# Optimization experiments

Hardware: AMD Instinct MI355X
Metric: run time of the kernel (lower is better)

The kernel has to match this reference:

```python
import jax, jax.numpy as jnp
import numpy as np

B, C_IN, C_OUT, H, K = 64, 64, 128, 1855, 6


def setup_inputs() -> dict:
    key = jax.random.key(0)
    k1, k2, k3, k4 = jax.random.split(key, 4)
    x = jax.random.normal(k1, (B, C_IN, H), dtype=jnp.float32)
    # neighbor table [H, K]; valid indices first, -1 padding at the end
    neighbors = jax.random.randint(k2, (H, K), 0, H)
    n_boundary = H // 10
    neighbors = neighbors.at[:n_boundary, K - 2:].set(-1)
    weight_center = jax.random.normal(k3, (C_OUT, C_IN), dtype=jnp.float32) / np.sqrt(C_IN).astype(np.float32)
    weight_neighbors = jax.random.normal(k4, (C_OUT, C_IN, K), dtype=jnp.float32) / np.sqrt(C_IN * K).astype(np.float32)
    bias = jnp.zeros((C_OUT,), dtype=jnp.float32)
    return {
        "x": x,
        "neighbors": neighbors,
        "weight_center": weight_center,
        "weight_neighbors": weight_neighbors,
        "bias": bias,
    }


def reference(x, neighbors, weight_center, weight_neighbors, bias):
    # x: [B, C_in, H]; neighbors: [H, K] with -1 = invalid (valid-first ordering)
    mask = neighbors >= 0                               # [H, K]
    idx = jnp.where(mask, neighbors, 0)                 # safe gather indices
    gathered = x[:, :, idx] * mask.astype(x.dtype)[None, None, :, :]  # [B, C_in, H, K]
    center = jnp.einsum('bch,oc->boh', x, weight_center)              # [B, C_out, H]
    neigh = jnp.einsum('bchk,ock->boh', gathered, weight_neighbors)   # [B, C_out, H]
    counts = (1 + mask.sum(axis=-1)).astype(x.dtype)                  # [H]
    return (center + neigh) / counts[None, None, :] + bias[None, :, None]
```

## Files before the change

kernel.cpp:

```cpp
#include <hip/hip_runtime.h>
#include <stdint.h>

typedef __bf16 bf16x8 __attribute__((ext_vector_type(8)));
typedef float floatx4 __attribute__((ext_vector_type(4)));
typedef unsigned int u32x4 __attribute__((ext_vector_type(4)));
typedef unsigned short u16;
typedef unsigned int u32;

#define CIN   64
#define COUT  128
#define H_    1855
#define KNB   6
#define KTOT  448
#define NSTEPS 14

#define HLROW 2064
#define BUFSZ 33024
#define STCP  36

#define WP_OFF   ((size_t)H_ * 4096 * 2)
#define CINV_OFF (WP_OFF + (size_t)COUT * KTOT * 2)
#define ZERO_OFF (CINV_OFF + 7424)

#define PIN4(v) asm volatile("" : "+v"(v))

typedef __attribute__((address_space(1))) unsigned int as1_u32;
typedef __attribute__((address_space(3))) unsigned int as3_u32;
static __device__ __forceinline__ void ld16_to_lds(const void* g, void* l) {
    __builtin_amdgcn_global_load_lds((const as1_u32*)g, (as3_u32*)l, 16, 0, 0);
}

static __device__ inline u16 f32_to_bf16(float f) {
    u32 u = __float_as_uint(f);
    u32 r = (u + 0x7FFFu + ((u >> 16) & 1u)) >> 16;
    return (u16)r;
}

__global__ __launch_bounds__(256) void k_transpose(const float* __restrict__ x,
                                                   u16* __restrict__ xt3) {
    __shared__ u16 tile[64][65];
    int h0  = blockIdx.x * 64;
    int bc0 = blockIdx.y * 64;
    int lane = threadIdx.x & 63;
    int rowq = threadIdx.x >> 6;
    int h = h0 + lane;
    bool hv = h < H_;
#pragma unroll
    for (int i = 0; i < 16; ++i) {
        int row = i * 4 + rowq;
        u16 v = 0;
        if (hv) v = f32_to_bf16(x[(size_t)(bc0 + row) * H_ + h]);
        tile[row][lane] = v;
    }
    __syncthreads();
#pragma unroll
    for (int i = 0; i < 16; ++i) {
        int hr = i * 4 + rowq;
        int hh = h0 + hr;
        if (hh < H_) xt3[(size_t)hh * 4096 + bc0 + lane] = tile[lane][hr];
    }
}

__global__ __launch_bounds__(256) void k_pack(const float* __restrict__ wc,
                                              const float* __restrict__ wn,
                                              const int* __restrict__ nbr,
                                              u16* __restrict__ wp,
                                              float* __restrict__ cInvG,
                                              u32* __restrict__ zeroPg) {
    int tg = blockIdx.x * 256 + threadIdx.x;
    if (tg < 64) zeroPg[tg] = 0u;
    if (tg < H_) {
        int cnt = 1;
#pragma unroll
        for (int j = 0; j < KNB; ++j) cnt += (nbr[tg * KNB + j] >= 0) ? 1 : 0;
        cInvG[tg] = 1.0f / (float)cnt;
    }
    if (tg >= COUT * KTOT) return;
    int o = tg / KTOT;
    int rem = tg - o * KTOT;
    int s = rem >> 6, c = rem & 63;
    float v = (s == 0) ? wc[o * CIN + c]
                       : wn[(o * CIN + c) * KNB + (s - 1)];
    wp[tg] = f32_to_bf16(v);
}

static __device__ __forceinline__ void stage_tile(
    const u16* __restrict__ xt3, const int* __restrict__ nbr,
    const char* __restrict__ zeroPg, char* bufB,
    int h0t, int b0, int wave, int lane) {
    int lane16 = lane & 15;
    int ssub   = lane >> 4;
    int bl     = lane16 >> 3;
    int chunk  = lane16 & 7;
#pragma unroll
    for (int i = 0; i < 8; ++i) {
        int hlL = i & 3;
        int sg  = i >> 2;
        int hl  = wave * 4 + hlL;
        int s   = sg * 4 + ssub;
        int hh  = h0t + hl;
        int hcl = hh < H_ ? hh : 0;
        int sidx = (s >= 1 && s <= 6) ? (s - 1) : 0;
        int nv  = nbr[hcl * KNB + sidx];
        int src = (s == 0) ? hcl : nv;
        bool valid = (hh < H_) && (s <= 6) && (src >= 0);
        const char* gp = valid
            ? (const char*)(xt3 + (size_t)src * 4096 + (b0 + bl) * 64 + chunk * 8)
            : (zeroPg + lane16 * 16);
        ld16_to_lds(gp, bufB + hl * HLROW + sg * 1024);
    }
}

__global__ __launch_bounds__(256, 2) void k_main(const u16* __restrict__ xt3,
                                                 const u16* __restrict__ wp,
                                                 const int* __restrict__ nbr,
                                                 const float* __restrict__ bias,
                                                 const float* __restrict__ cInvG,
                                                 const char* __restrict__ zeroPg,
                                                 float* __restrict__ out) {
    __shared__ __align__(16) char LDS[2 * BUFSZ];

    int tid  = threadIdx.x;
    int g    = blockIdx.x;
    int bp   = g & 31;
    int hs   = g >> 5;
    int b0   = bp * 2;
    int h0   = hs * 64;

    int lane = tid & 63;
    int wave = tid >> 6;
    int col  = lane & 15;
    int quad = lane >> 4;
    int m0w  = wave * 32;

    u32x4 afrag[2][NSTEPS];
#pragma unroll
    for (int mt = 0; mt < 2; ++mt) {
        int o = m0w + mt * 16 + col;
#pragma unroll
        for (int kk = 0; kk < NSTEPS; ++kk)
            afrag[mt][kk] = *(const u32x4*)(wp + o * KTOT + kk * 32 + quad * 8);
    }
#pragma unroll
    for (int mt = 0; mt < 2; ++mt)
#pragma unroll
        for (int kk = 0; kk < NSTEPS; ++kk)
            PIN4(afrag[mt][kk]);

    float biasv[2][4];
#pragma unroll
    for (int mt = 0; mt < 2; ++mt)
#pragma unroll
        for (int r = 0; r < 4; ++r)
            biasv[mt][r] = bias[m0w + mt * 16 + quad * 4 + r];

    int rb0 = col * HLROW + quad * 16;
    int rb1 = rb0 + 128;

    stage_tile(xt3, nbr, zeroPg, LDS, h0, b0, wave, lane);

#pragma unroll
    for (int tt = 0; tt < 4; ++tt) {
        int h0t = h0 + tt * 16;
        char* cur = LDS + (tt & 1) * BUFSZ;

        __syncthreads();

        if (tt < 3)
            stage_tile(xt3, nbr, zeroPg, LDS + ((tt + 1) & 1) * BUFSZ,
                       h0t + 16, b0, wave, lane);

        floatx4 acc[2][2];
#pragma unroll
        for (int mt = 0; mt < 2; ++mt)
#pragma unroll
            for (int nt = 0; nt < 2; ++nt)
                acc[mt][nt] = (floatx4){0.0f, 0.0f, 0.0f, 0.0f};

#pragma unroll
        for (int kk = 0; kk < NSTEPS; ++kk) {
            int koff = (kk >> 1) * 256 + (kk & 1) * 64;
            bf16x8 bf0 = *(const bf16x8*)(cur + rb0 + koff);
            bf16x8 bf1 = *(const bf16x8*)(cur + rb1 + koff);
            bf16x8 a0 = __builtin_bit_cast(bf16x8, afrag[0][kk]);
            bf16x8 a1 = __builtin_bit_cast(bf16x8, afrag[1][kk]);
            acc[0][0] = __builtin_amdgcn_mfma_f32_16x16x32_bf16(a0, bf0, acc[0][0], 0, 0, 0);
            acc[1][0] = __builtin_amdgcn_mfma_f32_16x16x32_bf16(a1, bf0, acc[1][0], 0, 0, 0);
            acc[0][1] = __builtin_amdgcn_mfma_f32_16x16x32_bf16(a0, bf1, acc[0][1], 0, 0, 0);
            acc[1][1] = __builtin_amdgcn_mfma_f32_16x16x32_bf16(a1, bf1, acc[1][1], 0, 0, 0);
        }

        __syncthreads();

        float* stC = (float*)cur;
        int hEp = h0t + col;
        float ic = cInvG[hEp < H_ ? hEp : 0];
#pragma unroll
        for (int mt = 0; mt < 2; ++mt)
#pragma unroll
            for (int nt = 0; nt < 2; ++nt)
#pragma unroll
                for (int r = 0; r < 4; ++r) {
                    int o = m0w + mt * 16 + quad * 4 + r;
                    stC[o * STCP + nt * 16 + col] = acc[mt][nt][r] * ic + biasv[mt][r];
                }
        int n5 = lane & 31, q2 = lane >> 5;
        int colS = n5 & 15, ntS = n5 >> 4;
        int hS = h0t + colS;
        bool hv = hS < H_;
        size_t obase = ((size_t)(b0 + ntS) * COUT) * H_ + hS;
#pragma unroll
        for (int rr = 0; rr < 16; ++rr) {
            int o = m0w + rr * 2 + q2;
            if (hv) out[obase + (size_t)o * H_] = stC[o * STCP + n5];
        }
    }
}

extern "C" void kernel_launch(void* const* d_in, const int* in_sizes, int n_in,
                              void* d_out, int out_size, void* d_ws, size_t ws_size,
                              hipStream_t stream) {
    const float* x    = (const float*)d_in[0];
    const int*   nbr  = (const int*)d_in[1];
    const float* wc   = (const float*)d_in[2];
    const float* wn   = (const float*)d_in[3];
    const float* bias = (const float*)d_in[4];

    u16*   xt3    = (u16*)d_ws;
    u16*   wp     = (u16*)((char*)d_ws + WP_OFF);
    float* cInvG  = (float*)((char*)d_ws + CINV_OFF);
    u32*   zeroPg = (u32*)((char*)d_ws + ZERO_OFF);

    k_pack<<<dim3((COUT * KTOT + 255) / 256), dim3(256), 0, stream>>>(
        wc, wn, nbr, wp, cInvG, zeroPg);
    k_transpose<<<dim3(29, 64), dim3(256), 0, stream>>>(x, xt3);
    k_main<<<dim3(928), dim3(256), 0, stream>>>(
        xt3, wp, nbr, bias, cInvG, (const char*)zeroPg, (float*)d_out);
}
```

Baseline: 140.3 us.

## Precompute gather offsets, hand-schedule staging with partial waits, vectorize transpose stores

k_pack now builds a per-hexagon table of byte offsets for the center and neighbor rows, with a sentinel for invalid entries, so k_main no longer computes gather addresses from the neighbor table inside its loop. k_main preloads all offsets and inverse counts into registers. It runs an explicit software pipeline with manual waitcnt barriers, including a partial vmcnt wait that keeps the next stage's loads in flight, raises wave priority around the MFMA loop, and batches the epilogue over two tiles through a swizzled LDS staging area for wider coalesced output stores. The transpose kernel now writes 16-byte vectors instead of 2-byte stores. The cost is higher register pressure and fragile hand-written waitcnt counts.

```diff
diff --git a/kernel.cpp b/kernel.cpp
--- a/kernel.cpp
+++ b/kernel.cpp
@@ -5,6 +5,7 @@
 typedef float floatx4 __attribute__((ext_vector_type(4)));
 typedef unsigned int u32x4 __attribute__((ext_vector_type(4)));
 typedef unsigned short u16;
+typedef unsigned short u16x8 __attribute__((ext_vector_type(8)));
 typedef unsigned int u32;
 
 #define CIN   64
@@ -16,11 +17,12 @@
 
 #define HLROW 2064
 #define BUFSZ 33024
-#define STCP  36
-
-#define WP_OFF   ((size_t)H_ * 4096 * 2)
-#define CINV_OFF (WP_OFF + (size_t)COUT * KTOT * 2)
-#define ZERO_OFF (CINV_OFF + 7424)
+
+#define WP_OFF     ((size_t)H_ * 4096 * 2)
+#define CINV_OFF   (WP_OFF + (size_t)COUT * KTOT * 2)
+#define ZERO_OFF   (CINV_OFF + 7424)
+#define SRCOFF_OFF (ZERO_OFF + 1024)
+#define INVOFF 0xFFFFFFFFu
 
 #define PIN4(v) asm volatile("" : "+v"(v))
 
@@ -41,8 +43,9 @@
     __shared__ u16 tile[64][65];
     int h0  = blockIdx.x * 64;
     int bc0 = blockIdx.y * 64;
-    int lane = threadIdx.x & 63;
-    int rowq = threadIdx.x >> 6;
+    int tid  = threadIdx.x;
+    int lane = tid & 63;
+    int rowq = tid >> 6;
     int h = h0 + lane;
     bool hv = h < H_;
 #pragma unroll
@@ -53,11 +56,17 @@
         tile[row][lane] = v;
     }
     __syncthreads();
-#pragma unroll
-    for (int i = 0; i < 16; ++i) {
-        int hr = i * 4 + rowq;
-        int hh = h0 + hr;
-        if (hh < H_) xt3[(size_t)hh * 4096 + bc0 + lane] = tile[lane][hr];
+    int bg = tid & 7;
+    int hb = tid >> 3;
+#pragma unroll
+    for (int ii = 0; ii < 2; ++ii) {
+        int hl = ii * 32 + hb;
+        int hh = h0 + hl;
+        u16x8 v;
+#pragma unroll
+        for (int j = 0; j < 8; ++j) v[j] = tile[bg * 8 + j][hl];
+        if (hh < H_)
+            *(u16x8*)(xt3 + (size_t)hh * 4096 + bc0 + bg * 8) = v;
     }
 }
 
@@ -66,7 +75,8 @@
                                               const int* __restrict__ nbr,
                                               u16* __restrict__ wp,
                                               float* __restrict__ cInvG,
-                                              u32* __restrict__ zeroPg) {
+                                              u32* __restrict__ zeroPg,
+                                              u32* __restrict__ srcOff) {
     int tg = blockIdx.x * 256 + threadIdx.x;
     if (tg < 64) zeroPg[tg] = 0u;
     if (tg < H_) {
@@ -74,6 +84,16 @@
 #pragma unroll
         for (int j = 0; j < KNB; ++j) cnt += (nbr[tg * KNB + j] >= 0) ? 1 : 0;
         cInvG[tg] = 1.0f / (float)cnt;
+    }
+    if (tg < H_ * 8) {
+        int h = tg >> 3, s = tg & 7;
+        u32 e;
+        if (s == 0) e = (u32)h * 8192u;
+        else if (s <= 6) {
+            int n = nbr[h * KNB + (s - 1)];
+            e = (n >= 0) ? (u32)n * 8192u : INVOFF;
+        } else e = INVOFF;
+        srcOff[tg] = e;
     }
     if (tg >= COUT * KTOT) return;
     int o = tg / KTOT;
@@ -84,46 +104,18 @@
     wp[tg] = f32_to_bf16(v);
 }
 
-static __device__ __forceinline__ void stage_tile(
-    const u16* __restrict__ xt3, const int* __restrict__ nbr,
-    const char* __restrict__ zeroPg, char* bufB,
-    int h0t, int b0, int wave, int lane) {
-    int lane16 = lane & 15;
-    int ssub   = lane >> 4;
-    int bl     = lane16 >> 3;
-    int chunk  = lane16 & 7;
-#pragma unroll
-    for (int i = 0; i < 8; ++i) {
-        int hlL = i & 3;
-        int sg  = i >> 2;
-        int hl  = wave * 4 + hlL;
-        int s   = sg * 4 + ssub;
-        int hh  = h0t + hl;
-        int hcl = hh < H_ ? hh : 0;
-        int sidx = (s >= 1 && s <= 6) ? (s - 1) : 0;
-        int nv  = nbr[hcl * KNB + sidx];
-        int src = (s == 0) ? hcl : nv;
-        bool valid = (hh < H_) && (s <= 6) && (src >= 0);
-        const char* gp = valid
-            ? (const char*)(xt3 + (size_t)src * 4096 + (b0 + bl) * 64 + chunk * 8)
-            : (zeroPg + lane16 * 16);
-        ld16_to_lds(gp, bufB + hl * HLROW + sg * 1024);
-    }
-}
-
 __global__ __launch_bounds__(256, 2) void k_main(const u16* __restrict__ xt3,
                                                  const u16* __restrict__ wp,
-                                                 const int* __restrict__ nbr,
                                                  const float* __restrict__ bias,
                                                  const float* __restrict__ cInvG,
-                                                 const char* __restrict__ zeroPg,
+                                                 const u32* __restrict__ srcOff,
                                                  float* __restrict__ out) {
     __shared__ __align__(16) char LDS[2 * BUFSZ];
 
     int tid  = threadIdx.x;
-    int g    = blockIdx.x;
-    int bp   = g & 31;
-    int hs   = g >> 5;
+    int gbl  = blockIdx.x;
+    int bp   = gbl & 31;
+    int hs   = gbl >> 5;
     int b0   = bp * 2;
     int h0   = hs * 64;
 
@@ -132,6 +124,12 @@
     int col  = lane & 15;
     int quad = lane >> 4;
     int m0w  = wave * 32;
+    int lane16 = lane & 15;
+    int ssub = lane >> 4;
+    int bl   = lane16 >> 3;
+    int chunk = lane16 & 7;
+
+    const char* xb = (const char*)xt3;
 
     u32x4 afrag[2][NSTEPS];
 #pragma unroll
@@ -154,67 +152,117 @@
         for (int r = 0; r < 4; ++r)
             biasv[mt][r] = bias[m0w + mt * 16 + quad * 4 + r];
 
+    float icv[4];
+#pragma unroll
+    for (int t = 0; t < 4; ++t) {
+        int hic = h0 + t * 16 + col;
+        icv[t] = cInvG[hic < H_ ? hic : 0];
+    }
+
+    u32 colOff = (u32)((b0 + bl) * 128 + chunk * 16);
+    u32 zOff   = (u32)ZERO_OFF + (u32)(lane16 * 16);
+    u32 offs[4][8];
+#pragma unroll
+    for (int t = 0; t < 4; ++t)
+#pragma unroll
+        for (int i = 0; i < 8; ++i) {
+            int hh = h0 + t * 16 + wave * 4 + (i & 3);
+            int s  = (i >> 2) * 4 + ssub;
+            u32 e = (hh < H_) ? srcOff[hh * 8 + s] : INVOFF;
+            offs[t][i] = (e == INVOFF) ? zOff : (e + colOff);
+        }
+
     int rb0 = col * HLROW + quad * 16;
     int rb1 = rb0 + 128;
-
-    stage_tile(xt3, nbr, zeroPg, LDS, h0, b0, wave, lane);
-
-#pragma unroll
-    for (int tt = 0; tt < 4; ++tt) {
-        int h0t = h0 + tt * 16;
-        char* cur = LDS + (tt & 1) * BUFSZ;
-
-        __syncthreads();
-
-        if (tt < 3)
-            stage_tile(xt3, nbr, zeroPg, LDS + ((tt + 1) & 1) * BUFSZ,
-                       h0t + 16, b0, wave, lane);
-
-        floatx4 acc[2][2];
-#pragma unroll
-        for (int mt = 0; mt < 2; ++mt)
-#pragma unroll
-            for (int nt = 0; nt < 2; ++nt)
-                acc[mt][nt] = (floatx4){0.0f, 0.0f, 0.0f, 0.0f};
-
-#pragma unroll
-        for (int kk = 0; kk < NSTEPS; ++kk) {
-            int koff = (kk >> 1) * 256 + (kk & 1) * 64;
-            bf16x8 bf0 = *(const bf16x8*)(cur + rb0 + koff);
-            bf16x8 bf1 = *(const bf16x8*)(cur + rb1 + koff);
-            bf16x8 a0 = __builtin_bit_cast(bf16x8, afrag[0][kk]);
-            bf16x8 a1 = __builtin_bit_cast(bf16x8, afrag[1][kk]);
-            acc[0][0] = __builtin_amdgcn_mfma_f32_16x16x32_bf16(a0, bf0, acc[0][0], 0, 0, 0);
-            acc[1][0] = __builtin_amdgcn_mfma_f32_16x16x32_bf16(a1, bf0, acc[1][0], 0, 0, 0);
-            acc[0][1] = __builtin_amdgcn_mfma_f32_16x16x32_bf16(a0, bf1, acc[0][1], 0, 0, 0);
-            acc[1][1] = __builtin_amdgcn_mfma_f32_16x16x32_bf16(a1, bf1, acc[1][1], 0, 0, 0);
-        }
-
-        __syncthreads();
-
-        float* stC = (float*)cur;
-        int hEp = h0t + col;
-        float ic = cInvG[hEp < H_ ? hEp : 0];
-#pragma unroll
-        for (int mt = 0; mt < 2; ++mt)
-#pragma unroll
-            for (int nt = 0; nt < 2; ++nt)
-#pragma unroll
-                for (int r = 0; r < 4; ++r) {
-                    int o = m0w + mt * 16 + quad * 4 + r;
-                    stC[o * STCP + nt * 16 + col] = acc[mt][nt][r] * ic + biasv[mt][r];
-                }
-        int n5 = lane & 31, q2 = lane >> 5;
-        int colS = n5 & 15, ntS = n5 >> 4;
-        int hS = h0t + colS;
-        bool hv = hS < H_;
-        size_t obase = ((size_t)(b0 + ntS) * COUT) * H_ + hS;
-#pragma unroll
-        for (int rr = 0; rr < 16; ++rr) {
-            int o = m0w + rr * 2 + q2;
-            if (hv) out[obase + (size_t)o * H_] = stC[o * STCP + n5];
-        }
-    }
+    char* buf0 = LDS;
+    char* buf1 = LDS + BUFSZ;
+    float* E = (float*)(LDS + BUFSZ);
+
+#define STAGE(t, bufp) do {                                                   \
+    char* _d = (bufp) + (wave * 4) * HLROW;                                   \
+    _Pragma("unroll")                                                         \
+    for (int _i = 0; _i < 8; ++_i)                                            \
+        ld16_to_lds(xb + offs[t][_i], _d + (_i & 3) * HLROW + (_i >> 2) * 1024); \
+} while (0)
+
+#define COMPUTE(accv, bufp) do {                                              \
+    _Pragma("unroll") for (int _m = 0; _m < 2; ++_m)                          \
+    _Pragma("unroll") for (int _n = 0; _n < 2; ++_n)                          \
+        accv[_m][_n] = (floatx4){0.0f, 0.0f, 0.0f, 0.0f};                     \
+    __builtin_amdgcn_s_setprio(1);                                            \
+    _Pragma("unroll")                                                         \
+    for (int kk = 0; kk < NSTEPS; ++kk) {                                     \
+        int koff = (kk >> 1) * 256 + (kk & 1) * 64;                           \
+        bf16x8 bfa = *(const bf16x8*)((bufp) + rb0 + koff);                   \
+        bf16x8 bfb = *(const bf16x8*)((bufp) + rb1 + koff);                   \
+        bf16x8 a0 = __builtin_bit_cast(bf16x8, afrag[0][kk]);                 \
+        bf16x8 a1 = __builtin_bit_cast(bf16x8, afrag[1][kk]);                 \
+        accv[0][0] = __builtin_amdgcn_mfma_f32_16x16x32_bf16(a0, bfa, accv[0][0], 0, 0, 0); \
+        accv[1][0] = __builtin_amdgcn_mfma_f32_16x16x32_bf16(a1, bfa, accv[1][0], 0, 0, 0); \
+        accv[0][1] = __builtin_amdgcn_mfma_f32_16x16x32_bf16(a0, bfb, accv[0][1], 0, 0, 0); \
+        accv[1][1] = __builtin_amdgcn_mfma_f32_16x16x32_bf16(a1, bfb, accv[1][1], 0, 0, 0); \
+    }                                                                         \
+    __builtin_amdgcn_s_setprio(0);                                            \
+} while (0)
+
+#define EPIW(pp, t, accv) do {                                                \
+    float _ic = icv[(pp) * 2 + (t)];                                          \
+    _Pragma("unroll") for (int _m = 0; _m < 2; ++_m)                          \
+    _Pragma("unroll") for (int _n = 0; _n < 2; ++_n)                          \
+    _Pragma("unroll") for (int _r = 0; _r < 4; ++_r) {                        \
+        int _row = m0w + _m * 16 + quad * 4 + _r;                             \
+        int _idx = ((_n) * 32 + (t) * 16 + col) ^ (quad << 3);                \
+        E[_row * 64 + _idx] = accv[_m][_n][_r] * _ic + biasv[_m][_r];         \
+    }                                                                         \
+} while (0)
+
+#define EPIS(pp) do {                                                         \
+    int _h5 = lane & 31, _g = lane >> 5;                                      \
+    int _hh = h0 + (pp) * 32 + _h5;                                           \
+    bool _hv = _hh < H_;                                                      \
+    size_t _ob = (size_t)(b0 + _g) * ((size_t)COUT * H_)                      \
+               + (size_t)m0w * H_ + _hh;                                      \
+    _Pragma("unroll")                                                         \
+    for (int _j = 0; _j < 32; ++_j) {                                         \
+        float _v = E[(m0w + _j) * 64 + ((_g * 32 + _h5) ^ (((_j >> 2) & 3) << 3))]; \
+        if (_hv) out[_ob + (size_t)_j * H_] = _v;                             \
+    }                                                                         \
+} while (0)
+
+#define ABAR0()  do { asm volatile("s_waitcnt vmcnt(0) lgkmcnt(0)" ::: "memory");  __builtin_amdgcn_s_barrier(); } while (0)
+#define ABAR32() do { asm volatile("s_waitcnt vmcnt(32) lgkmcnt(0)" ::: "memory"); __builtin_amdgcn_s_barrier(); } while (0)
+#define BBAR()   do { asm volatile("s_waitcnt lgkmcnt(0)" ::: "memory");           __builtin_amdgcn_s_barrier(); } while (0)
+
+    floatx4 accA[2][2], accB[2][2];
+
+    STAGE(0, buf0);
+    ABAR0();
+    STAGE(1, buf1);
+    COMPUTE(accA, buf0);
+    ABAR0();
+    STAGE(2, buf0);
+    COMPUTE(accB, buf1);
+    BBAR();
+    EPIW(0, 0, accA);
+    EPIW(0, 1, accB);
+    EPIS(0);
+    ABAR32();
+    STAGE(3, buf1);
+    COMPUTE(accA, buf0);
+    ABAR0();
+    COMPUTE(accB, buf1);
+    BBAR();
+    EPIW(1, 0, accA);
+    EPIW(1, 1, accB);
+    EPIS(1);
+
+#undef STAGE
+#undef COMPUTE
+#undef EPIW
+#undef EPIS
+#undef ABAR0
+#undef ABAR32
+#undef BBAR
 }
 
 extern "C" void kernel_launch(void* const* d_in, const int* in_sizes, int n_in,
@@ -230,10 +278,11 @@
     u16*   wp     = (u16*)((char*)d_ws + WP_OFF);
     float* cInvG  = (float*)((char*)d_ws + CINV_OFF);
     u32*   zeroPg = (u32*)((char*)d_ws + ZERO_OFF);
+    u32*   srcOff = (u32*)((char*)d_ws + SRCOFF_OFF);
 
     k_pack<<<dim3((COUT * KTOT + 255) / 256), dim3(256), 0, stream>>>(
-        wc, wn, nbr, wp, cInvG, zeroPg);
+        wc, wn, nbr, wp, cInvG, zeroPg, srcOff);
     k_transpose<<<dim3(29, 64), dim3(256), 0, stream>>>(x, xt3);
     k_main<<<dim3(928), dim3(256), 0, stream>>>(
-        xt3, wp, nbr, bias, cInvG, (const char*)zeroPg, (float*)d_out);
-}
+        xt3, wp, bias, cInvG, srcOff, (float*)d_out);
+}
```

Result: faster. 134.5 us (-4.1%).
